# Kernel optimization log

Measured on AMD Instinct MI355X. Metric: run time of the kernel, lower is better.

## Reference

```python
import jax, jax.numpy as jnp
from jax import lax
import numpy as np

N = 2000      # num_nodes
T_IN = 24
T_OUT = 12
B = 32
H = 64        # hidden_dim
D = 10        # embed_dim / adapt_dim
K = 2         # cheb_k
C_IN = 1


def setup_inputs() -> dict:
    key = jax.random.key(0)
    ks = jax.random.split(key, 13)
    s = 0.1  # xavier-ish scale
    f32 = jnp.float32
    return {
        "x": jax.random.normal(ks[0], (B, T_IN, N), f32),
        "node_emb": jax.random.normal(ks[1], (N, D), f32) * s,
        "adapt_emb": jax.random.normal(ks[2], (N, D), f32) * s,
        # layer 0 NAPL weight/bias pools (gate: 2H out, candidate: H out)
        "Wg0": jax.random.normal(ks[3], (D, K, C_IN + H, 2 * H), f32) * s,
        "bg0": jax.random.normal(ks[4], (D, 2 * H), f32) * s,
        "Wc0": jax.random.normal(ks[5], (D, K, C_IN + H, H), f32) * s,
        "bc0": jax.random.normal(ks[6], (D, H), f32) * s,
        # layer 1 pools (input is hidden_dim)
        "Wg1": jax.random.normal(ks[7], (D, K, 2 * H, 2 * H), f32) * s,
        "bg1": jax.random.normal(ks[8], (D, 2 * H), f32) * s,
        "Wc1": jax.random.normal(ks[9], (D, K, 2 * H, H), f32) * s,
        "bc1": jax.random.normal(ks[10], (D, H), f32) * s,
        # 1x1 conv head == per-node linear hidden -> T_out
        "head_w": jax.random.normal(ks[11], (T_OUT, H), f32) * s,
        "head_b": jnp.zeros((T_OUT,), f32),
    }


def reference(x, node_emb, adapt_emb, Wg0, bg0, Wc0, bc0, Wg1, bg1, Wc1, bc1,
              head_w, head_b):
    Bn, T, Nn = x.shape
    # adaptive adjacency: row-softmax(relu(E E^T)); no prior -> A_used = A_adapt
    A = jax.nn.softmax(jax.nn.relu(adapt_emb @ adapt_emb.T), axis=-1)
    supports = jnp.stack([jnp.eye(Nn, dtype=x.dtype), A])  # (K, N, N)

    def napl(Wp, bp):
        # node-adaptive parameter learning: per-node weights/biases
        W = jnp.einsum('nd,dkio->nkio', node_emb, Wp)  # (N, K, Cin, Cout)
        b = node_emb @ bp                              # (N, Cout)
        return W, b

    p = [napl(Wg0, bg0), napl(Wc0, bc0), napl(Wg1, bg1), napl(Wc1, bc1)]

    def gconv(inp, W, b):
        # inp: (B, N, C)
        xg = jnp.einsum('knm,bmc->bknc', supports, inp)      # (B, K, N, C)
        return jnp.einsum('bkni,nkio->bno', xg, W) + b       # (B, N, Cout)

    def cell(xt, h, gW, gb, cW, cb):
        zr = jax.nn.sigmoid(gconv(jnp.concatenate([xt, h], -1), gW, gb))
        z, r = jnp.split(zr, 2, axis=-1)
        hc = jnp.tanh(gconv(jnp.concatenate([xt, r * h], -1), cW, cb))
        return z * h + (1.0 - z) * hc

    def step(carry, xt):
        h0, h1 = carry
        h0 = cell(xt, h0, p[0][0], p[0][1], p[1][0], p[1][1])
        h1 = cell(h0, h1, p[2][0], p[2][1], p[3][0], p[3][1])
        return (h0, h1), None

    xs = jnp.transpose(x[..., None], (1, 0, 2, 3))  # (T, B, N, 1)
    h0 = jnp.zeros((Bn, Nn, H), x.dtype)
    h1 = jnp.zeros((Bn, Nn, H), x.dtype)
    (h0, h1), _ = lax.scan(step, (h0, h1), xs)

    # 1x1 conv head on (B, H, N, 1) == per-node linear: (B, T_out, N)
    y = jnp.einsum('bnh,oh->bon', h1, head_w) + head_b[None, :, None]
    return y
```

## Files before the change

kernel.cpp:

```cpp
#include <hip/hip_runtime.h>
#include <math.h>

#define NN 2000
#define BB 32
#define TT 24
#define T_OUT 12
#define HH 64
#define DD 10
#define NP 2048
#define BC 2048

typedef unsigned short ushort_t;
typedef __bf16 bf16x8 __attribute__((ext_vector_type(8)));
typedef float f32x4 __attribute__((ext_vector_type(4)));

__device__ __forceinline__ float sigmoidf_(float x) { return 1.f / (1.f + expf(-x)); }

__device__ __forceinline__ ushort_t f2bf(float f) {
    unsigned int u = __float_as_uint(f);
    unsigned int r = (u + 0x7FFFu + ((u >> 16) & 1u)) >> 16;
    return (ushort_t)r;
}
__device__ __forceinline__ float bf2f(ushort_t s) {
    return __uint_as_float(((unsigned int)s) << 16);
}

__device__ __forceinline__ void glld16(const ushort_t* g, ushort_t* lds) {
    __builtin_amdgcn_global_load_lds(
        (const __attribute__((address_space(1))) char*)g,
        (__attribute__((address_space(3))) char*)lds, 16, 0, 0);
}

__device__ __forceinline__ unsigned lds_off(const void* p) {
    return (unsigned)(size_t)(__attribute__((address_space(3))) const char*)p;
}

constexpr size_t SZ_NPNP2 = (size_t)NP * NP * 2;
constexpr size_t SZ_ST4   = (size_t)NN * BC * 4;
constexpr size_t SZ_NPB2  = (size_t)NP * BC * 2;

constexpr size_t ABF_OFF  = 0;
constexpr size_t H0F_OFF  = ABF_OFF + SZ_NPNP2;
constexpr size_t H1F_OFF  = H0F_OFF + SZ_ST4;
constexpr size_t ZF_OFF   = H1F_OFF + SZ_ST4;
constexpr size_t H0B_OFF  = ZF_OFF + SZ_ST4;
constexpr size_t H1B_OFF  = H0B_OFF + SZ_NPB2;
constexpr size_t RHB_OFF  = H1B_OFF + SZ_NPB2;
constexpr size_t AH0_OFF  = RHB_OFF + SZ_NPB2;
constexpr size_t AHX_OFF  = AH0_OFF + SZ_NPB2;
constexpr size_t AXF_OFF  = AHX_OFF + SZ_NPB2;
constexpr size_t BTG0_OFF = AXF_OFF + (size_t)BB * TT * NN * 4;
constexpr size_t BTC0_OFF = BTG0_OFF + (size_t)DD * 128 * 128 * 2;
constexpr size_t BTG1_OFF = BTC0_OFF + (size_t)DD * 64 * 128 * 2;
constexpr size_t BTC1_OFF = BTG1_OFF + (size_t)DD * 128 * 256 * 2;
constexpr size_t WS_TOP   = BTC1_OFF + (size_t)DD * 64 * 256 * 2;

__global__ __launch_bounds__(256) void compute_A_kernel(const float* __restrict__ E,
                                                        float* __restrict__ A) {
    const int row = blockIdx.x;
    const int tid = threadIdx.x;
    float er[DD];
#pragma unroll
    for (int d = 0; d < DD; ++d) er[d] = E[row * DD + d];
    __shared__ float red[8];

    float lmax = -1e30f;
    for (int c = tid; c < NN; c += 256) {
        float s = 0.f;
#pragma unroll
        for (int d = 0; d < DD; ++d) s += er[d] * E[c * DD + d];
        s = fmaxf(s, 0.f);
        A[(size_t)row * NN + c] = s;
        lmax = fmaxf(lmax, s);
    }
#pragma unroll
    for (int o = 32; o > 0; o >>= 1) lmax = fmaxf(lmax, __shfl_down(lmax, o, 64));
    if ((tid & 63) == 0) red[tid >> 6] = lmax;
    __syncthreads();
    const float rmax = fmaxf(fmaxf(red[0], red[1]), fmaxf(red[2], red[3]));
    __syncthreads();

    float lsum = 0.f;
    for (int c = tid; c < NN; c += 256) {
        float v = expf(A[(size_t)row * NN + c] - rmax);
        A[(size_t)row * NN + c] = v;
        lsum += v;
    }
#pragma unroll
    for (int o = 32; o > 0; o >>= 1) lsum += __shfl_down(lsum, o, 64);
    if ((tid & 63) == 0) red[4 + (tid >> 6)] = lsum;
    __syncthreads();
    const float inv = 1.f / (red[4] + red[5] + red[6] + red[7]);
    for (int c = tid; c < NN; c += 256) A[(size_t)row * NN + c] *= inv;
}

__global__ __launch_bounds__(256) void convert_A(const float* __restrict__ Af,
                                                 ushort_t* __restrict__ Ab) {
    size_t idx = (size_t)blockIdx.x * 256 + threadIdx.x;
    int r = (int)(idx >> 11), c = (int)(idx & 2047);
    float v = (r < NN && c < NN) ? Af[(size_t)r * NN + c] : 0.f;
    Ab[idx] = f2bf(v);
}

__global__ __launch_bounds__(256) void ax2_kernel(const float* __restrict__ A,
                                                  const float* __restrict__ x,
                                                  float* __restrict__ Ax) {
    __shared__ float As[64][66];
    __shared__ float xs[64][98];
    const int n0 = blockIdx.x * 64;
    const int b0 = blockIdx.y * 4;
    const int tid = threadIdx.x;
    const int tr = tid >> 4, tc = tid & 15;
    float acc[4][6] = {};

    for (int m0 = 0; m0 < NN; m0 += 64) {
#pragma unroll
        for (int l = 0; l < 16; ++l) {
            int idx = tid + l * 256;
            int mm = idx & 63, r = idx >> 6;
            int n = n0 + r, m = m0 + mm;
            As[mm][r] = (n < NN && m < NN) ? A[(size_t)n * NN + m] : 0.f;
        }
#pragma unroll
        for (int l = 0; l < 24; ++l) {
            int idx = tid + l * 256;
            int mm = idx & 63, col = idx >> 6;
            int m = m0 + mm;
            int bl = col / 24, t = col - bl * 24;
            xs[mm][col] = (m < NN) ? x[((size_t)(b0 + bl) * TT + t) * NN + m] : 0.f;
        }
        __syncthreads();
#pragma unroll 4
        for (int mm = 0; mm < 64; ++mm) {
            float2 a01 = *(const float2*)&As[mm][tr * 4];
            float2 a23 = *(const float2*)&As[mm][tr * 4 + 2];
            float xv[6];
            *(float2*)&xv[0] = *(const float2*)&xs[mm][tc * 6];
            *(float2*)&xv[2] = *(const float2*)&xs[mm][tc * 6 + 2];
            *(float2*)&xv[4] = *(const float2*)&xs[mm][tc * 6 + 4];
            float av[4] = {a01.x, a01.y, a23.x, a23.y};
#pragma unroll
            for (int i = 0; i < 4; ++i)
#pragma unroll
                for (int j = 0; j < 6; ++j) acc[i][j] += av[i] * xv[j];
        }
        __syncthreads();
    }
#pragma unroll
    for (int i = 0; i < 4; ++i) {
        const int n = n0 + tr * 4 + i;
        if (n < NN) {
#pragma unroll
            for (int j = 0; j < 6; ++j) {
                int col = tc * 6 + j;
                int bl = col / 24, t = col - bl * 24;
                Ax[((size_t)(b0 + bl) * TT + t) * NN + n] = acc[i][j];
            }
        }
    }
}

__global__ __launch_bounds__(256) void gemm_trb(const ushort_t* __restrict__ Ab,
                                                const ushort_t* __restrict__ H0,
                                                ushort_t* __restrict__ Y0,
                                                const ushort_t* __restrict__ H1,
                                                ushort_t* __restrict__ Y1) {
    __shared__ __align__(16) ushort_t As[64 * 64];
    __shared__ __align__(16) ushort_t Bs[2][32 * 128];
    const ushort_t* __restrict__ H = (blockIdx.z == 0) ? H0 : H1;
    ushort_t* __restrict__ Y = (blockIdx.z == 0) ? Y0 : Y1;
    const int tid = threadIdx.x;
    const int w = tid >> 6, l = tid & 63, lr = l & 15, lg = l >> 4;
    const int n0 = blockIdx.x * 64, j0 = blockIdx.y * 128;
    f32x4 acc[4][2] = {};

    const int arow = tid >> 3, asl = tid & 7;
    const unsigned bs0 = lds_off(Bs);
    const unsigned btr_b[2] = {
        bs0 + 2u * ((unsigned)(w * 2 + 0) * 512 + (unsigned)lg * 128 + (unsigned)lr),
        bs0 + 2u * ((unsigned)(w * 2 + 1) * 512 + (unsigned)lg * 128 + (unsigned)lr)};

    for (int ks = 0; ks < NP / 64; ++ks) {
        const int k0 = ks * 64;
#pragma unroll
        for (int p = 0; p < 2; ++p) {
            const int idx = p * 256 + tid;
            const int row = idx >> 3, sl = idx & 7;
            glld16(Ab + (size_t)(n0 + row) * NP + k0 + ((sl ^ (row & 7)) << 3),
                   (ushort_t*)((char*)As + idx * 16));
        }
#pragma unroll
        for (int p = 0; p < 4; ++p) {
            const int idx = p * 256 + tid;
            const int g = idx >> 9, li = idx & 511;
            const int row = k0 + g * 32 + ((li >> 3) & 7) * 4 + ((li >> 1) & 3);
            const int col = j0 + (li >> 6) * 16 + (li & 1) * 8;
            glld16(H + (size_t)row * BC + col,
                   (ushort_t*)((char*)Bs + g * 8192 + li * 16));
        }
        __syncthreads();

        bf16x8 av[2][4];
#pragma unroll
        for (int kk = 0; kk < 2; ++kk)
#pragma unroll
            for (int m = 0; m < 4; ++m) {
                const int rr = m * 16 + lr;
                av[kk][m] = *(const bf16x8*)&As[rr * 64 + (((kk * 4 + lg) ^ (rr & 7)) << 3)];
            }
        unsigned long long bq[2][2][2];
        asm volatile(
            "ds_read_b64_tr_b16 %0, %8 offset:0\n\t"
            "ds_read_b64_tr_b16 %1, %8 offset:128\n\t"
            "ds_read_b64_tr_b16 %2, %9 offset:0\n\t"
            "ds_read_b64_tr_b16 %3, %9 offset:128\n\t"
            "ds_read_b64_tr_b16 %4, %8 offset:8192\n\t"
            "ds_read_b64_tr_b16 %5, %8 offset:8320\n\t"
            "ds_read_b64_tr_b16 %6, %9 offset:8192\n\t"
            "ds_read_b64_tr_b16 %7, %9 offset:8320"
            : "=v"(bq[0][0][0]), "=v"(bq[0][0][1]), "=v"(bq[0][1][0]), "=v"(bq[0][1][1]),
              "=v"(bq[1][0][0]), "=v"(bq[1][0][1]), "=v"(bq[1][1][0]), "=v"(bq[1][1][1])
            : "v"(btr_b[0]), "v"(btr_b[1]));
        asm volatile("s_waitcnt lgkmcnt(0)" ::: "memory");
        __builtin_amdgcn_sched_barrier(0);
        bf16x8 bv[2][2];
#pragma unroll
        for (int kk = 0; kk < 2; ++kk)
#pragma unroll
            for (int nt = 0; nt < 2; ++nt) {
                union { unsigned long long q[2]; bf16x8 f; } u;
                u.q[0] = bq[kk][nt][0];
                u.q[1] = bq[kk][nt][1];
                bv[kk][nt] = u.f;
            }

#pragma unroll
        for (int kk = 0; kk < 2; ++kk)
#pragma unroll
            for (int m = 0; m < 4; ++m)
#pragma unroll
                for (int nt = 0; nt < 2; ++nt)
                    acc[m][nt] = __builtin_amdgcn_mfma_f32_16x16x32_bf16(av[kk][m], bv[kk][nt], acc[m][nt], 0, 0, 0);
        __syncthreads();
    }

#pragma unroll
    for (int m = 0; m < 4; ++m)
#pragma unroll
        for (int r = 0; r < 4; ++r) {
            const int n = n0 + m * 16 + lg * 4 + r;
            if (n < NN) {
#pragma unroll
                for (int nt = 0; nt < 2; ++nt)
                    Y[(size_t)n * BC + j0 + w * 32 + nt * 16 + lr] = f2bf(acc[m][nt][r]);
            }
        }
}

template <int CI, int CO, bool L0>
__global__ __launch_bounds__(256) void prepW(const float* __restrict__ Wp,
                                             ushort_t* __restrict__ Bt) {
    constexpr int K = L0 ? 128 : 256;
    const int idx = blockIdx.x * 256 + threadIdx.x;
    if (idx >= DD * CO * K) return;
    const int d = idx / (CO * K);
    const int rem = idx - d * CO * K;
    const int o = rem / K;
    const int k = rem - o * K;
    const int s = k >> 6, c = k & 63;
    const int kk = L0 ? s : (s & 1);
    const int i = L0 ? (1 + c) : ((s >> 1) * 64 + c);
    Bt[idx] = f2bf(Wp[((size_t)(d * 2 + kk) * CI + i) * CO + o]);
}

template <int NSEGS, int CO, bool GATE, bool HASX>
__global__ __launch_bounds__(256) void napl2(
    const ushort_t* __restrict__ Bt, const float* __restrict__ bp,
    const float* __restrict__ emb, const float* __restrict__ WxPool,
    const ushort_t* __restrict__ s0p, const ushort_t* __restrict__ s1p,
    const ushort_t* __restrict__ s2p, const ushort_t* __restrict__ s3p,
    const float* __restrict__ xv, const float* __restrict__ axv,
    const float* hf, float* __restrict__ zf,
    ushort_t* __restrict__ outb, float* outf, int t) {
    constexpr int K = NSEGS * 64;
    constexpr int NT = (CO == 128) ? 2 : 1;
    constexpr int NHALF = NSEGS / 2;
    __shared__ __align__(16) ushort_t As[NSEGS * 64 * 64];
    const int tid = threadIdx.x;
    const int w = tid >> 6, l = tid & 63, lr = l & 15, lg = l >> 4;
    const int n0 = blockIdx.x * 2;
    const int ob = w * (16 * NT);
    const ushort_t* segs[4] = {s0p, s1p, s2p, s3p};

#pragma unroll
    for (int s = 0; s < NSEGS; ++s) {
        const ushort_t* sp = segs[s];
#pragma unroll
        for (int p = 0; p < 2; ++p) {
            const int idx = p * 256 + tid;
            const int row = idx >> 3, c16 = idx & 7;
            glld16(sp + (size_t)(n0 + (row >> 5)) * BC + (row & 31) * 64 +
                       ((c16 ^ (row & 7)) << 3),
                   (ushort_t*)((char*)As + s * 8192 + idx * 16));
        }
    }
    __syncthreads();

    f32x4 OUT[4][NT] = {};
#pragma unroll 1
    for (int hf2 = 0; hf2 < NHALF; ++hf2) {
        bf16x8 av[4][4];
#pragma unroll
        for (int c = 0; c < 4; ++c) {
            const int s = hf2 * 2 + (c >> 1);
            const int kin = (c & 1) * 32 + lg * 8;
#pragma unroll
            for (int m = 0; m < 4; ++m) {
                const int rr = m * 16 + lr;
                av[c][m] = *(const bf16x8*)&As[s * 4096 + rr * 64 + (kin ^ ((rr & 7) << 3))];
            }
        }
#pragma unroll 1
        for (int d = 0; d < DD; ++d) {
            const ushort_t* btd = Bt + (size_t)d * CO * K;
            const float ea = emb[n0 * DD + d];
            const float eb = emb[(n0 + 1) * DD + d];
            f32x4 P[4][NT] = {};
#pragma unroll
            for (int c = 0; c < 4; ++c) {
                const int kg = (hf2 * 2 + (c >> 1)) * 64 + (c & 1) * 32 + lg * 8;
                bf16x8 bv[NT];
#pragma unroll
                for (int nt = 0; nt < NT; ++nt)
                    bv[nt] = *(const bf16x8*)&btd[(size_t)(ob + nt * 16 + lr) * K + kg];
#pragma unroll
                for (int m = 0; m < 4; ++m)
#pragma unroll
                    for (int nt = 0; nt < NT; ++nt)
                        P[m][nt] = __builtin_amdgcn_mfma_f32_16x16x32_bf16(av[c][m], bv[nt], P[m][nt], 0, 0, 0);
            }
#pragma unroll
            for (int m = 0; m < 4; ++m) {
                const float e = (m < 2) ? ea : eb;
#pragma unroll
                for (int nt = 0; nt < NT; ++nt)
#pragma unroll
                    for (int r = 0; r < 4; ++r)
                        OUT[m][nt][r] += e * P[m][nt][r];
            }
        }
    }

    float bias[2][NT];
#pragma unroll
    for (int nd = 0; nd < 2; ++nd)
#pragma unroll
        for (int nt = 0; nt < NT; ++nt) {
            float s_ = 0.f;
#pragma unroll
            for (int d = 0; d < DD; ++d)
                s_ += emb[(n0 + nd) * DD + d] * bp[d * CO + ob + nt * 16 + lr];
            bias[nd][nt] = s_;
        }
    float wx[2][2][NT] = {};
    if (HASX) {
#pragma unroll
        for (int kk = 0; kk < 2; ++kk)
#pragma unroll
            for (int nd = 0; nd < 2; ++nd)
#pragma unroll
                for (int nt = 0; nt < NT; ++nt) {
                    float s_ = 0.f;
#pragma unroll
                    for (int d = 0; d < DD; ++d)
                        s_ += emb[(n0 + nd) * DD + d] *
                              WxPool[(size_t)(d * 2 + kk) * 65 * CO + ob + nt * 16 + lr];
                    wx[kk][nd][nt] = s_;
                }
    }

#pragma unroll
    for (int m = 0; m < 4; ++m) {
        const int nd = m >> 1;
        const int n = n0 + nd;
#pragma unroll
        for (int r = 0; r < 4; ++r) {
            const int row = m * 16 + lg * 4 + r;
            const int b = row & 31;
            const size_t nb = (size_t)n * BC + b * 64;
            float xt = 0.f, axt = 0.f;
            if (HASX) {
                xt = xv[((size_t)b * TT + t) * NN + n];
                axt = axv[((size_t)b * TT + t) * NN + n];
            }
#pragma unroll
            for (int nt = 0; nt < NT; ++nt) {
                const int o = ob + nt * 16 + lr;
                float val = OUT[m][nt][r] + bias[nd][nt];
                if (HASX) val += xt * wx[0][nd][nt] + axt * wx[1][nd][nt];
                if (GATE) {
                    const float sg = sigmoidf_(val);
                    if (ob < 64) {
                        zf[nb + o] = sg;
                    } else {
                        outb[nb + (o - 64)] = f2bf(sg * hf[nb + (o - 64)]);
                    }
                } else {
                    const float hc = tanhf(val);
                    const float z = zf[nb + o];
                    const float hn = z * hf[nb + o] + (1.f - z) * hc;
                    outf[nb + o] = hn;
                    outb[nb + o] = f2bf(hn);
                }
            }
        }
    }
}

__global__ __launch_bounds__(256) void head_kernel(const float* __restrict__ h1,
                                                   const float* __restrict__ hw,
                                                   const float* __restrict__ hb,
                                                   float* __restrict__ y) {
    __shared__ float wl[T_OUT * HH];
    const int tid = threadIdx.x;
    for (int idx = tid; idx < T_OUT * HH; idx += 256) wl[idx] = hw[idx];
    __syncthreads();
    const int gi = blockIdx.x * 256 + tid;
    if (gi >= BB * NN) return;
    const int b = gi / NN, n = gi % NN;
    float acc[T_OUT];
#pragma unroll
    for (int ot = 0; ot < T_OUT; ++ot) acc[ot] = hb[ot];
    for (int h = 0; h < HH; ++h) {
        float v = h1[(size_t)n * BC + b * 64 + h];
#pragma unroll
        for (int ot = 0; ot < T_OUT; ++ot) acc[ot] += v * wl[ot * HH + h];
    }
#pragma unroll
    for (int ot = 0; ot < T_OUT; ++ot)
        y[((size_t)b * T_OUT + ot) * NN + n] = acc[ot];
}

extern "C" void kernel_launch(void* const* d_in, const int* in_sizes, int n_in,
                              void* d_out, int out_size, void* d_ws, size_t ws_size,
                              hipStream_t stream) {
    const float* x = (const float*)d_in[0];
    const float* node_emb = (const float*)d_in[1];
    const float* adapt_emb = (const float*)d_in[2];
    const float* Wg0 = (const float*)d_in[3];
    const float* bg0 = (const float*)d_in[4];
    const float* Wc0 = (const float*)d_in[5];
    const float* bc0 = (const float*)d_in[6];
    const float* Wg1 = (const float*)d_in[7];
    const float* bg1 = (const float*)d_in[8];
    const float* Wc1 = (const float*)d_in[9];
    const float* bc1 = (const float*)d_in[10];
    const float* head_w = (const float*)d_in[11];
    const float* head_b = (const float*)d_in[12];
    float* y = (float*)d_out;

    char* ws = (char*)d_ws;
    ushort_t* Abf  = (ushort_t*)(ws + ABF_OFF);
    float* h0f = (float*)(ws + H0F_OFF);
    float* h1f = (float*)(ws + H1F_OFF);
    float* zf  = (float*)(ws + ZF_OFF);
    ushort_t* h0b = (ushort_t*)(ws + H0B_OFF);
    ushort_t* h1b = (ushort_t*)(ws + H1B_OFF);
    ushort_t* rhb = (ushort_t*)(ws + RHB_OFF);
    ushort_t* Ah0 = (ushort_t*)(ws + AH0_OFF);
    ushort_t* AhX = (ushort_t*)(ws + AHX_OFF);
    float* Axf = (float*)(ws + AXF_OFF);
    ushort_t* Btg0 = (ushort_t*)(ws + BTG0_OFF);
    ushort_t* Btc0 = (ushort_t*)(ws + BTC0_OFF);
    ushort_t* Btg1 = (ushort_t*)(ws + BTG1_OFF);
    ushort_t* Btc1 = (ushort_t*)(ws + BTC1_OFF);
    float* Af32 = zf;

    hipMemsetAsync(h0f, 0, SZ_ST4, stream);
    hipMemsetAsync(h1f, 0, SZ_ST4, stream);
    hipMemsetAsync(h0b, 0, SZ_NPB2, stream);
    hipMemsetAsync(h1b, 0, SZ_NPB2, stream);
    hipMemsetAsync(rhb, 0, SZ_NPB2, stream);
    hipMemsetAsync(Ah0, 0, SZ_NPB2, stream);
    hipMemsetAsync(AhX, 0, SZ_NPB2, stream);

    compute_A_kernel<<<NN, 256, 0, stream>>>(adapt_emb, Af32);
    ax2_kernel<<<dim3(32, 8), 256, 0, stream>>>(Af32, x, Axf);
    convert_A<<<(NP * NP) / 256, 256, 0, stream>>>(Af32, Abf);
    prepW<65, 128, true><<<(DD * 128 * 128 + 255) / 256, 256, 0, stream>>>(Wg0, Btg0);
    prepW<65, 64, true><<<(DD * 64 * 128 + 255) / 256, 256, 0, stream>>>(Wc0, Btc0);
    prepW<128, 128, false><<<(DD * 128 * 256 + 255) / 256, 256, 0, stream>>>(Wg1, Btg1);
    prepW<128, 64, false><<<(DD * 64 * 256 + 255) / 256, 256, 0, stream>>>(Wc1, Btc1);

    const dim3 gG1(NP / 64, NP / 128, 1);
    const dim3 gG2(NP / 64, NP / 128, 2);
    const int gN = NN * BB / 64;

    for (int t = 0; t < TT; ++t) {
        napl2<2, 128, true, true><<<gN, 256, 0, stream>>>(
            Btg0, bg0, node_emb, Wg0, h0b, Ah0, h0b, h0b, x, Axf, h0f, zf, rhb, nullptr, t);
        gemm_trb<<<gG1, 256, 0, stream>>>(Abf, rhb, AhX, rhb, AhX);
        napl2<2, 64, false, true><<<gN, 256, 0, stream>>>(
            Btc0, bc0, node_emb, Wc0, rhb, AhX, rhb, rhb, x, Axf, h0f, zf, h0b, h0f, t);
        gemm_trb<<<gG2, 256, 0, stream>>>(Abf, h0b, Ah0, h1b, AhX);
        napl2<4, 128, true, false><<<gN, 256, 0, stream>>>(
            Btg1, bg1, node_emb, nullptr, h0b, Ah0, h1b, AhX, nullptr, nullptr, h1f, zf, rhb, nullptr, t);
        gemm_trb<<<gG1, 256, 0, stream>>>(Abf, rhb, AhX, rhb, AhX);
        napl2<4, 64, false, false><<<gN, 256, 0, stream>>>(
            Btc1, bc1, node_emb, nullptr, h0b, Ah0, rhb, AhX, nullptr, nullptr, h1f, zf, h1b, h1f, t);
    }

    head_kernel<<<(BB * NN + 255) / 256, 256, 0, stream>>>(h1f, head_w, head_b, y);
}
```

Measured before the change: 9.026 ms.

## Software-pipeline recurrent steps by merging independent GEMM and NAPL launches

Restructures the time loop so that the layer-1 gate GEMM of step t runs in the same launch as the layer-0 gate NAPL of step t+1. Likewise, the layer-0 candidate GEMM of step t+1 shares a launch with the layer-1 candidate NAPL of step t. The gemm and napl bodies become device functions dispatched by block index inside combined kernels. Double-buffered z/r·h and A·X buffers separate the two in-flight steps. This cuts launches per step from seven to five and fills the GPU with more concurrent blocks. In exchange it needs extra workspace, falls back to the old path when the workspace is too small, and uses larger shared memory per block in the merged kernels.

```diff
diff --git a/kernel.cpp b/kernel.cpp
--- a/kernel.cpp
+++ b/kernel.cpp
@@ -54,6 +54,10 @@
 constexpr size_t BTG1_OFF = BTC0_OFF + (size_t)DD * 64 * 128 * 2;
 constexpr size_t BTC1_OFF = BTG1_OFF + (size_t)DD * 128 * 256 * 2;
 constexpr size_t WS_TOP   = BTC1_OFF + (size_t)DD * 64 * 256 * 2;
+constexpr size_t ZF1_OFF  = WS_TOP;
+constexpr size_t RHB1_OFF = ZF1_OFF + SZ_ST4;
+constexpr size_t AHY_OFF  = RHB1_OFF + SZ_NPB2;
+constexpr size_t TOP_PIPE = AHY_OFF + SZ_NPB2;
 
 __global__ __launch_bounds__(256) void compute_A_kernel(const float* __restrict__ E,
                                                         float* __restrict__ A) {
@@ -160,21 +164,18 @@
     }
 }
 
-__global__ __launch_bounds__(256) void gemm_trb(const ushort_t* __restrict__ Ab,
-                                                const ushort_t* __restrict__ H0,
-                                                ushort_t* __restrict__ Y0,
-                                                const ushort_t* __restrict__ H1,
-                                                ushort_t* __restrict__ Y1) {
-    __shared__ __align__(16) ushort_t As[64 * 64];
-    __shared__ __align__(16) ushort_t Bs[2][32 * 128];
-    const ushort_t* __restrict__ H = (blockIdx.z == 0) ? H0 : H1;
-    ushort_t* __restrict__ Y = (blockIdx.z == 0) ? Y0 : Y1;
+
+__device__ __forceinline__ void gemm_body(int bx, int by,
+                                          const ushort_t* __restrict__ Ab,
+                                          const ushort_t* __restrict__ H,
+                                          ushort_t* __restrict__ Y, char* smem) {
+    ushort_t* As = (ushort_t*)smem;
+    ushort_t* Bs = (ushort_t*)(smem + 8192);
     const int tid = threadIdx.x;
     const int w = tid >> 6, l = tid & 63, lr = l & 15, lg = l >> 4;
-    const int n0 = blockIdx.x * 64, j0 = blockIdx.y * 128;
+    const int n0 = bx * 64, j0 = by * 128;
     f32x4 acc[4][2] = {};
 
-    const int arow = tid >> 3, asl = tid & 7;
     const unsigned bs0 = lds_off(Bs);
     const unsigned btr_b[2] = {
         bs0 + 2u * ((unsigned)(w * 2 + 0) * 512 + (unsigned)lg * 128 + (unsigned)lr),
@@ -257,24 +258,9 @@
         }
 }
 
-template <int CI, int CO, bool L0>
-__global__ __launch_bounds__(256) void prepW(const float* __restrict__ Wp,
-                                             ushort_t* __restrict__ Bt) {
-    constexpr int K = L0 ? 128 : 256;
-    const int idx = blockIdx.x * 256 + threadIdx.x;
-    if (idx >= DD * CO * K) return;
-    const int d = idx / (CO * K);
-    const int rem = idx - d * CO * K;
-    const int o = rem / K;
-    const int k = rem - o * K;
-    const int s = k >> 6, c = k & 63;
-    const int kk = L0 ? s : (s & 1);
-    const int i = L0 ? (1 + c) : ((s >> 1) * 64 + c);
-    Bt[idx] = f2bf(Wp[((size_t)(d * 2 + kk) * CI + i) * CO + o]);
-}
-
 template <int NSEGS, int CO, bool GATE, bool HASX>
-__global__ __launch_bounds__(256) void napl2(
+__device__ __forceinline__ void napl_body(
+    int bid, char* smem,
     const ushort_t* __restrict__ Bt, const float* __restrict__ bp,
     const float* __restrict__ emb, const float* __restrict__ WxPool,
     const ushort_t* __restrict__ s0p, const ushort_t* __restrict__ s1p,
@@ -285,10 +271,10 @@
     constexpr int K = NSEGS * 64;
     constexpr int NT = (CO == 128) ? 2 : 1;
     constexpr int NHALF = NSEGS / 2;
-    __shared__ __align__(16) ushort_t As[NSEGS * 64 * 64];
+    ushort_t* As = (ushort_t*)smem;
     const int tid = threadIdx.x;
     const int w = tid >> 6, l = tid & 63, lr = l & 15, lg = l >> 4;
-    const int n0 = blockIdx.x * 2;
+    const int n0 = bid * 2;
     const int ob = w * (16 * NT);
     const ushort_t* segs[4] = {s0p, s1p, s2p, s3p};
 
@@ -417,6 +403,82 @@
     }
 }
 
+
+__global__ __launch_bounds__(256) void gemm_trb(const ushort_t* __restrict__ Ab,
+                                                const ushort_t* __restrict__ H0,
+                                                ushort_t* __restrict__ Y0,
+                                                const ushort_t* __restrict__ H1,
+                                                ushort_t* __restrict__ Y1) {
+    __shared__ __align__(16) char smem[24576];
+    gemm_body(blockIdx.x, blockIdx.y, Ab,
+              (blockIdx.z == 0) ? H0 : H1, (blockIdx.z == 0) ? Y0 : Y1, smem);
+}
+
+template <int NSEGS, int CO, bool GATE, bool HASX>
+__global__ __launch_bounds__(256) void napl2(
+    const ushort_t* __restrict__ Bt, const float* __restrict__ bp,
+    const float* __restrict__ emb, const float* __restrict__ WxPool,
+    const ushort_t* __restrict__ s0p, const ushort_t* __restrict__ s1p,
+    const ushort_t* __restrict__ s2p, const ushort_t* __restrict__ s3p,
+    const float* __restrict__ xv, const float* __restrict__ axv,
+    const float* hf, float* __restrict__ zf,
+    ushort_t* __restrict__ outb, float* outf, int t) {
+    __shared__ __align__(16) char smem[NSEGS * 8192];
+    napl_body<NSEGS, CO, GATE, HASX>(blockIdx.x, smem, Bt, bp, emb, WxPool,
+                                     s0p, s1p, s2p, s3p, xv, axv, hf, zf, outb, outf, t);
+}
+
+__global__ __launch_bounds__(256) void mergeA_k(
+    const ushort_t* __restrict__ Abf, const ushort_t* __restrict__ Hg,
+    ushort_t* __restrict__ Yg,
+    const ushort_t* __restrict__ Bt, const float* __restrict__ bp,
+    const float* __restrict__ emb, const float* __restrict__ Wx,
+    const ushort_t* __restrict__ s0, const ushort_t* __restrict__ s1,
+    const float* __restrict__ xv, const float* __restrict__ axv,
+    const float* hf, float* __restrict__ zf, ushort_t* __restrict__ outb, int t) {
+    __shared__ __align__(16) char smem[24576];
+    const int g = blockIdx.x;
+    if (g < 512)
+        gemm_body(g & 31, g >> 5, Abf, Hg, Yg, smem);
+    else
+        napl_body<2, 128, true, true>(g - 512, smem, Bt, bp, emb, Wx,
+                                      s0, s1, s0, s0, xv, axv, hf, zf, outb, nullptr, t);
+}
+
+__global__ __launch_bounds__(256) void mergeB_k(
+    const ushort_t* __restrict__ Abf, const ushort_t* __restrict__ Hg,
+    ushort_t* __restrict__ Yg,
+    const ushort_t* __restrict__ Bt, const float* __restrict__ bp,
+    const float* __restrict__ emb,
+    const ushort_t* __restrict__ s0, const ushort_t* __restrict__ s1,
+    const ushort_t* __restrict__ s2, const ushort_t* __restrict__ s3,
+    const float* hf, float* __restrict__ zf,
+    ushort_t* __restrict__ outb, float* outf, int t) {
+    __shared__ __align__(16) char smem[32768];
+    const int g = blockIdx.x;
+    if (g < 512)
+        gemm_body(g & 31, g >> 5, Abf, Hg, Yg, smem);
+    else
+        napl_body<4, 64, false, false>(g - 512, smem, Bt, bp, emb, nullptr,
+                                       s0, s1, s2, s3, nullptr, nullptr, hf, zf, outb, outf, t);
+}
+
+template <int CI, int CO, bool L0>
+__global__ __launch_bounds__(256) void prepW(const float* __restrict__ Wp,
+                                             ushort_t* __restrict__ Bt) {
+    constexpr int K = L0 ? 128 : 256;
+    const int idx = blockIdx.x * 256 + threadIdx.x;
+    if (idx >= DD * CO * K) return;
+    const int d = idx / (CO * K);
+    const int rem = idx - d * CO * K;
+    const int o = rem / K;
+    const int k = rem - o * K;
+    const int s = k >> 6, c = k & 63;
+    const int kk = L0 ? s : (s & 1);
+    const int i = L0 ? (1 + c) : ((s >> 1) * 64 + c);
+    Bt[idx] = f2bf(Wp[((size_t)(d * 2 + kk) * CI + i) * CO + o]);
+}
+
 __global__ __launch_bounds__(256) void head_kernel(const float* __restrict__ h1,
                                                    const float* __restrict__ hw,
                                                    const float* __restrict__ hb,
@@ -476,6 +538,8 @@
     ushort_t* Btc1 = (ushort_t*)(ws + BTC1_OFF);
     float* Af32 = zf;
 
+    const bool pipe = (ws_size >= TOP_PIPE);
+
     hipMemsetAsync(h0f, 0, SZ_ST4, stream);
     hipMemsetAsync(h1f, 0, SZ_ST4, stream);
     hipMemsetAsync(h0b, 0, SZ_NPB2, stream);
@@ -496,18 +560,51 @@
     const dim3 gG2(NP / 64, NP / 128, 2);
     const int gN = NN * BB / 64;
 
-    for (int t = 0; t < TT; ++t) {
+    if (pipe) {
+        float* zf0 = zf;
+        ushort_t* rhb0 = rhb;
+        float* zf1 = (float*)(ws + ZF1_OFF);
+        ushort_t* rhb1 = (ushort_t*)(ws + RHB1_OFF);
+        ushort_t* AhY = (ushort_t*)(ws + AHY_OFF);
+        hipMemsetAsync(rhb1, 0, SZ_NPB2, stream);
+
         napl2<2, 128, true, true><<<gN, 256, 0, stream>>>(
-            Btg0, bg0, node_emb, Wg0, h0b, Ah0, h0b, h0b, x, Axf, h0f, zf, rhb, nullptr, t);
-        gemm_trb<<<gG1, 256, 0, stream>>>(Abf, rhb, AhX, rhb, AhX);
+            Btg0, bg0, node_emb, Wg0, h0b, Ah0, h0b, h0b, x, Axf, h0f, zf0, rhb0, nullptr, 0);
+        gemm_trb<<<gG1, 256, 0, stream>>>(Abf, rhb0, AhY, rhb0, AhY);
         napl2<2, 64, false, true><<<gN, 256, 0, stream>>>(
-            Btc0, bc0, node_emb, Wc0, rhb, AhX, rhb, rhb, x, Axf, h0f, zf, h0b, h0f, t);
+            Btc0, bc0, node_emb, Wc0, rhb0, AhY, rhb0, rhb0, x, Axf, h0f, zf0, h0b, h0f, 0);
         gemm_trb<<<gG2, 256, 0, stream>>>(Abf, h0b, Ah0, h1b, AhX);
         napl2<4, 128, true, false><<<gN, 256, 0, stream>>>(
-            Btg1, bg1, node_emb, nullptr, h0b, Ah0, h1b, AhX, nullptr, nullptr, h1f, zf, rhb, nullptr, t);
-        gemm_trb<<<gG1, 256, 0, stream>>>(Abf, rhb, AhX, rhb, AhX);
+            Btg1, bg1, node_emb, nullptr, h0b, Ah0, h1b, AhX, nullptr, nullptr, h1f, zf1, rhb1, nullptr, 0);
+
+        for (int t = 0; t < TT - 1; ++t) {
+            mergeA_k<<<1512, 256, 0, stream>>>(Abf, rhb1, AhX,
+                Btg0, bg0, node_emb, Wg0, h0b, Ah0, x, Axf, h0f, zf0, rhb0, t + 1);
+            mergeB_k<<<1512, 256, 0, stream>>>(Abf, rhb0, AhY,
+                Btc1, bc1, node_emb, h0b, Ah0, rhb1, AhX, h1f, zf1, h1b, h1f, t);
+            napl2<2, 64, false, true><<<gN, 256, 0, stream>>>(
+                Btc0, bc0, node_emb, Wc0, rhb0, AhY, rhb0, rhb0, x, Axf, h0f, zf0, h0b, h0f, t + 1);
+            gemm_trb<<<gG2, 256, 0, stream>>>(Abf, h0b, Ah0, h1b, AhX);
+            napl2<4, 128, true, false><<<gN, 256, 0, stream>>>(
+                Btg1, bg1, node_emb, nullptr, h0b, Ah0, h1b, AhX, nullptr, nullptr, h1f, zf1, rhb1, nullptr, t + 1);
+        }
+        gemm_trb<<<gG1, 256, 0, stream>>>(Abf, rhb1, AhX, rhb1, AhX);
         napl2<4, 64, false, false><<<gN, 256, 0, stream>>>(
-            Btc1, bc1, node_emb, nullptr, h0b, Ah0, rhb, AhX, nullptr, nullptr, h1f, zf, h1b, h1f, t);
+            Btc1, bc1, node_emb, nullptr, h0b, Ah0, rhb1, AhX, nullptr, nullptr, h1f, zf1, h1b, h1f, TT - 1);
+    } else {
+        for (int t = 0; t < TT; ++t) {
+            napl2<2, 128, true, true><<<gN, 256, 0, stream>>>(
+                Btg0, bg0, node_emb, Wg0, h0b, Ah0, h0b, h0b, x, Axf, h0f, zf, rhb, nullptr, t);
+            gemm_trb<<<gG1, 256, 0, stream>>>(Abf, rhb, AhX, rhb, AhX);
+            napl2<2, 64, false, true><<<gN, 256, 0, stream>>>(
+                Btc0, bc0, node_emb, Wc0, rhb, AhX, rhb, rhb, x, Axf, h0f, zf, h0b, h0f, t);
+            gemm_trb<<<gG2, 256, 0, stream>>>(Abf, h0b, Ah0, h1b, AhX);
+            napl2<4, 128, true, false><<<gN, 256, 0, stream>>>(
+                Btg1, bg1, node_emb, nullptr, h0b, Ah0, h1b, AhX, nullptr, nullptr, h1f, zf, rhb, nullptr, t);
+            gemm_trb<<<gG1, 256, 0, stream>>>(Abf, rhb, AhX, rhb, AhX);
+            napl2<4, 64, false, false><<<gN, 256, 0, stream>>>(
+                Btc1, bc1, node_emb, nullptr, h0b, Ah0, rhb, AhX, nullptr, nullptr, h1f, zf, h1b, h1f, t);
+        }
     }
 
     head_kernel<<<(BB * NN + 255) / 256, 256, 0, stream>>>(h1f, head_w, head_b, y);
```

After: 8.803 ms. -2.5%, faster.
